# Kernel optimization log

Measured on AMD Instinct MI355X. Metric: run time of the kernel, lower is better.

The kernel has to match this reference:

```python
import jax, jax.numpy as jnp
import numpy as np

N, E, B = 100000, 400000, 4096      # nodes, directed edges, graphs
P, d = 4, 49                        # phm_dim, per-component dim; D = P*d = 196
L = 3                               # message-passing layers
D1, D2 = 64, 32                     # downstream per-component dims (256/4, 128/4)


def setup_inputs():
    key = jax.random.key(0)
    ks = jax.random.split(key, 20)
    def nrm(k, shape, s=0.1):
        return jax.random.normal(k, shape, dtype=jnp.float32) * s
    return {
        "x": jax.random.randint(ks[0], (N, 9), 0, 119),
        "edge_index": jax.random.randint(ks[1], (2, E), 0, N),
        "edge_attr": jax.random.randint(ks[2], (E, 3), 0, 8),
        "batch": jnp.sort(jax.random.randint(ks[3], (N,), 0, B)),
        # encoders: summed categorical embeddings in hypercomplex form [*, P, d]
        "atom_emb": nrm(ks[4], (9, 119, P, d)),
        "bond_emb": nrm(ks[5], (L, 3, 8, P, d)),
        # per-layer PHM conv: contribution matrices A (phm rule) + component weights W
        "conv_A": nrm(ks[6], (L, P, P, P), 0.5),
        "conv_W": nrm(ks[7], (L, P, d, d)),
        "conv_b": jnp.zeros((L, P, d), jnp.float32),
        "mp_gamma": jnp.ones((L, P * d), jnp.float32),
        "mp_beta": jnp.zeros((L, P * d), jnp.float32),
        # soft-attention pooling: PHM linear + real transformer gate
        "pool_A": nrm(ks[8], (P, P, P), 0.5),
        "pool_W": nrm(ks[9], (P, d, d)),
        "pool_b": jnp.zeros((P, d), jnp.float32),
        "pool_rt_w": nrm(ks[10], (P,), 0.5),
        "pool_rt_b": jnp.zeros((d,), jnp.float32),
        # downstream PHM MLP 196 -> 256 -> 128 -> 4*1, then real trafo -> 1
        "dn_A": nrm(ks[11], (3, P, P, P), 0.5),
        "dn1_W": nrm(ks[12], (P, d, D1)),
        "dn1_b": jnp.zeros((P, D1), jnp.float32),
        "dn1_gamma": jnp.ones((P * D1,), jnp.float32),
        "dn1_beta": jnp.zeros((P * D1,), jnp.float32),
        "dn2_W": nrm(ks[13], (P, D1, D2)),
        "dn2_b": jnp.zeros((P, D2), jnp.float32),
        "dn2_gamma": jnp.ones((P * D2,), jnp.float32),
        "dn2_beta": jnp.zeros((P * D2,), jnp.float32),
        "dn3_W": nrm(ks[14], (P, D2, 1)),
        "dn3_b": jnp.zeros((P, 1), jnp.float32),
        "rt_w": nrm(ks[15], (P,), 0.5),
        "rt_b": jnp.zeros((1,), jnp.float32),
    }


def phm_linear(x, A, W, b):
    # PHM linear: y = x @ (sum_i kron(A_i, W_i)) + b, on [n, P, din] -> [n, P, dout]
    return jnp.einsum('nkp,ikj,ipq->njq', x, A, W) + b


def naive_bn(x, gamma, beta, eps=1e-5):
    # naive batch norm over the batch axis, per flattened hypercomplex feature
    n, p, dd = x.shape
    x2 = x.reshape(n, p * dd)
    mu = x2.mean(axis=0)
    var = x2.var(axis=0)
    x2 = (x2 - mu) * jax.lax.rsqrt(var + eps) * gamma + beta
    return x2.reshape(n, p, dd)


def reference(x, edge_index, edge_attr, batch, atom_emb, bond_emb,
              conv_A, conv_W, conv_b, mp_gamma, mp_beta,
              pool_A, pool_W, pool_b, pool_rt_w, pool_rt_b,
              dn_A, dn1_W, dn1_b, dn1_gamma, dn1_beta,
              dn2_W, dn2_b, dn2_gamma, dn2_beta, dn3_W, dn3_b, rt_w, rt_b):
    src, dst = edge_index[0], edge_index[1]
    # atom encoder: sum embeddings of 9 categorical features -> [N, P, d]
    h0 = atom_emb[jnp.arange(9), x].sum(axis=1)
    h = h0
    for l in range(L):  # small fixed layer count
        # bond encoder for this layer -> [E, P, d]
        e = bond_emb[l][jnp.arange(3), edge_attr].sum(axis=1)
        # message = x_j + e_ij (identity msg encoder); self-loop (zero edge feat) adds h
        m = h[src] + e
        agg = jax.ops.segment_sum(m, dst, num_segments=N) + h
        z = phm_linear(agg, conv_A[l], conv_W[l], conv_b[l])
        z = jax.nn.relu(naive_bn(z, mp_gamma[l], mp_beta[l]))
        h = z + h0  # skip-connect to first embedding (sc_type='first')
    # soft-attention pooling: real-valued sigmoid gate per node feature
    g = jax.nn.sigmoid(
        jnp.einsum('npk,p->nk', phm_linear(h, pool_A, pool_W, pool_b), pool_rt_w)
        + pool_rt_b)
    pooled = jax.ops.segment_sum(h * g[:, None, :], batch, num_segments=B)  # [B, P, d]
    # downstream PHM MLP with naive batch norm + relu
    z = jax.nn.relu(naive_bn(phm_linear(pooled, dn_A[0], dn1_W, dn1_b), dn1_gamma, dn1_beta))
    z = jax.nn.relu(naive_bn(phm_linear(z, dn_A[1], dn2_W, dn2_b), dn2_gamma, dn2_beta))
    o = phm_linear(z, dn_A[2], dn3_W, dn3_b)          # [B, P, 1]
    return jnp.einsum('npk,p->nk', o, rt_w) + rt_b    # [B, 1]
```

## Files before the change

kernel.cpp:

```cpp
#include <hip/hip_runtime.h>
#include <cstdint>
#include <cstddef>

#define N_NODES 100000
#define N_EDGES 400000
#define N_GRAPHS 4096
#define DF 196
#define DD 49
#define NPB 5
#define TST 200
#define WSLOT 14336
#define EST 232

#define AS1 __attribute__((address_space(1)))
#define AS3 __attribute__((address_space(3)))

typedef __bf16 bf16x8 __attribute__((ext_vector_type(8)));
typedef float f32x4 __attribute__((ext_vector_type(4)));

__device__ __forceinline__ unsigned short f2bf(float f) {
  unsigned int u = __float_as_uint(f);
  u = u + 0x7FFFu + ((u >> 16) & 1u);
  return (unsigned short)(u >> 16);
}
__device__ __forceinline__ float bf2f(unsigned short h) {
  return __uint_as_float(((unsigned int)h) << 16);
}

__global__ void convert_wfrag_kernel(const float* __restrict__ cA,
                                     const float* __restrict__ cW,
                                     unsigned short* __restrict__ wfrag) {
  int idx = blockIdx.x * blockDim.x + threadIdx.x;
  if (idx >= 3 * 100352) return;
  int l = idx / 100352;
  int r = idx - l * 100352;
  int ct = r / 7168; int r1 = r - ct * 7168;
  int ks = r1 / 1024; int r2 = r1 - ks * 1024;
  int h = r2 / 512;  int r3 = r2 - h * 512;
  int ln = r3 / 8;   int j = r3 - ln * 8;
  int col = ct * 16 + (ln & 15);
  int k = ks * 32 + (ln >> 4) * 8 + j;
  float v = 0.f;
  if (col < DF && k < DF) {
    int k4 = k / DD, p = k - (k / DD) * DD;
    int j4 = col / DD, q = col - (col / DD) * DD;
#pragma unroll
    for (int i = 0; i < 4; i++)
      v += cA[((l * 4 + i) * 4 + k4) * 4 + j4] * cW[((l * 4 + i) * DD + p) * DD + q];
  }
  unsigned short hi = f2bf(v);
  wfrag[idx] = (h == 0) ? hi : f2bf(v - bf2f(hi));
}

__global__ void setup_small_kernel(const float* __restrict__ bond, float* __restrict__ lut,
                                   const float* __restrict__ pA, const float* __restrict__ pW,
                                   const float* __restrict__ pb, const float* __restrict__ rtw,
                                   const float* __restrict__ rtb,
                                   unsigned short* __restrict__ wfragG,
                                   float* __restrict__ gbias,
                                   const float* __restrict__ dnA,
                                   const float* __restrict__ W1, const float* __restrict__ W2,
                                   const float* __restrict__ W3,
                                   float* __restrict__ M1, float* __restrict__ M2,
                                   float* __restrict__ M3) {
  int idx0 = blockIdx.x * blockDim.x + threadIdx.x;
  const int NL = 3 * 512 * DF;
  const int NGF = 28672;
  const int NB2 = 64;
  const int n1 = DF * 256, n2 = 256 * 128, n3 = 128 * 4;
  if (idx0 < NL) {
    int idx = idx0;
    int l = idx / (512 * DF);
    int r = idx - l * (512 * DF);
    int code = r / DF, c = r - (r / DF) * DF;
    int a0 = code & 7, a1 = (code >> 3) & 7, a2 = (code >> 6) & 7;
    lut[idx] = bond[((l * 3 + 0) * 8 + a0) * DF + c]
             + bond[((l * 3 + 1) * 8 + a1) * DF + c]
             + bond[((l * 3 + 2) * 8 + a2) * DF + c];
  } else if (idx0 < NL + NGF) {
    int idx = idx0 - NL;
    int ct = idx / 7168; int r1 = idx - ct * 7168;
    int ks = r1 / 1024; int r2 = r1 - ks * 1024;
    int h = r2 / 512;  int r3 = r2 - h * 512;
    int ln = r3 / 8;   int j = r3 - ln * 8;
    int col = ct * 16 + (ln & 15);
    int k = ks * 32 + (ln >> 4) * 8 + j;
    float v = 0.f;
    if (col < DD && k < DF) {
      int kp = k / DD, p = k - (k / DD) * DD;
#pragma unroll
      for (int i = 0; i < 4; i++) {
        float aw = 0.f;
#pragma unroll
        for (int j4 = 0; j4 < 4; j4++) aw += pA[(i * 4 + kp) * 4 + j4] * rtw[j4];
        v += aw * pW[(i * DD + p) * DD + col];
      }
    }
    unsigned short hi = f2bf(v);
    wfragG[idx] = (h == 0) ? hi : f2bf(v - bf2f(hi));
  } else if (idx0 < NL + NGF + NB2) {
    int q = idx0 - NL - NGF;
    if (q < DD) {
      float s = rtb[q];
#pragma unroll
      for (int j = 0; j < 4; j++) s += rtw[j] * pb[j * DD + q];
      gbias[q] = s;
    }
  } else if (idx0 < NL + NGF + NB2 + n1 + n2 + n3) {
    int idx = idx0 - NL - NGF - NB2;
    if (idx < n1) {
      int r = idx >> 8, c = idx & 255;
      int k = r / DD, p = r - (r / DD) * DD;
      int j = c >> 6, Q = c & 63;
      float s = 0.f;
#pragma unroll
      for (int i = 0; i < 4; i++) s += dnA[i * 16 + k * 4 + j] * W1[(i * DD + p) * 64 + Q];
      M1[idx] = s;
    } else if (idx < n1 + n2) {
      int m = idx - n1;
      int r = m >> 7, c = m & 127;
      int k = r >> 6, p = r & 63, j = c >> 5, q = c & 31;
      float s = 0.f;
#pragma unroll
      for (int i = 0; i < 4; i++) s += dnA[64 + i * 16 + k * 4 + j] * W2[(i * 64 + p) * 32 + q];
      M2[m] = s;
    } else {
      int m = idx - n1 - n2;
      int r = m >> 2, j = m & 3;
      int k = r >> 5, p = r & 31;
      float s = 0.f;
#pragma unroll
      for (int i = 0; i < 4; i++) s += dnA[128 + i * 16 + k * 4 + j] * W3[i * 32 + p];
      M3[m] = s;
    }
  }
}

__global__ void hist_kernel(const int* __restrict__ dst, int* __restrict__ counts) {
  int e = blockIdx.x * blockDim.x + threadIdx.x;
  if (e < N_EDGES) atomicAdd(&counts[dst[e]], 1);
}

__global__ void scan_local_kernel(const int* __restrict__ counts, int* __restrict__ offs,
                                  int* __restrict__ bsum) {
  __shared__ int sm[256];
  int tid = threadIdx.x;
  int gid = blockIdx.x * 256 + tid;
  int v = (gid < N_NODES) ? counts[gid] : 0;
  sm[tid] = v;
  __syncthreads();
  for (int d = 1; d < 256; d <<= 1) {
    int add = (tid >= d) ? sm[tid - d] : 0;
    __syncthreads();
    sm[tid] += add;
    __syncthreads();
  }
  if (gid < N_NODES) offs[gid] = sm[tid] - v;
  if (tid == 255) bsum[blockIdx.x] = sm[255];
}

__global__ void scan_bsum_kernel(int* __restrict__ bsum, int* __restrict__ bpre, int nb) {
  __shared__ int sm[512];
  int tid = threadIdx.x;
  int v = (tid < nb) ? bsum[tid] : 0;
  sm[tid] = v;
  __syncthreads();
  for (int d = 1; d < 512; d <<= 1) {
    int add = (tid >= d) ? sm[tid - d] : 0;
    __syncthreads();
    sm[tid] += add;
    __syncthreads();
  }
  if (tid < nb) bpre[tid] = sm[tid] - v;
}

__global__ void add_off_kernel(int* __restrict__ offs, const int* __restrict__ bpre) {
  int gid = blockIdx.x * blockDim.x + threadIdx.x;
  if (gid < N_NODES) offs[gid] += bpre[gid >> 8];
  if (gid == 0) offs[N_NODES] = N_EDGES;
}

__global__ void scatter_kernel(const int* __restrict__ src, const int* __restrict__ dst,
                               const int* __restrict__ ea, int* __restrict__ counts,
                               const int* __restrict__ offs,
                               unsigned int* __restrict__ sorted) {
  int e = blockIdx.x * blockDim.x + threadIdx.x;
  if (e >= N_EDGES) return;
  int d = dst[e];
  int code = ea[e * 3 + 0] | (ea[e * 3 + 1] << 3) | (ea[e * 3 + 2] << 6);
  int pos = offs[d] + atomicSub(&counts[d], 1) - 1;
  sorted[pos] = (unsigned int)src[e] | ((unsigned int)code << 17);
}

__global__ void sortseg_kernel(const int* __restrict__ offs,
                               unsigned int* __restrict__ sorted) {
  int n = blockIdx.x * blockDim.x + threadIdx.x;
  if (n >= N_NODES) return;
  int s = offs[n], e = offs[n + 1];
  for (int i = s + 1; i < e; i++) {
    unsigned int v = sorted[i];
    int j = i - 1;
    while (j >= s && sorted[j] > v) { sorted[j + 1] = sorted[j]; j--; }
    sorted[j + 1] = v;
  }
}

__global__ void atom_enc_kernel(const int* __restrict__ x, const float* __restrict__ emb,
                                float* __restrict__ h0) {
  int idx = blockIdx.x * blockDim.x + threadIdx.x;
  if (idx >= N_NODES * DF) return;
  int n = idx / DF;
  int c = idx - n * DF;
  float s = 0.f;
#pragma unroll
  for (int f = 0; f < 9; f++) {
    int xi = x[n * 9 + f];
    s += emb[(f * 119 + xi) * DF + c];
  }
  h0[idx] = s;
}

__global__ __launch_bounds__(256)
void agg_kernel(const float* __restrict__ h, const int* __restrict__ offs,
                const unsigned int* __restrict__ sorted, const float* __restrict__ lut,
                unsigned short* __restrict__ tH, unsigned short* __restrict__ tL) {
  int t = threadIdx.x;
  int i = t / 49, q = t - i * 49;
  if (i >= NPB) return;
  int node = blockIdx.x * NPB + i;
  if (node >= N_NODES) return;
  const float4* h4 = (const float4*)h;
  const float4* l4 = (const float4*)lut;
  float4 acc = h4[(size_t)node * 49 + q];
  int s = offs[node], e = offs[node + 1];
  for (int k = s; k < e; k++) {
    unsigned int se = sorted[k];
    int srcn = se & 0x1FFFF;
    int code = se >> 17;
    float4 hv = h4[(size_t)srcn * 49 + q];
    float4 lv = l4[(size_t)code * 49 + q];
    acc.x += hv.x + lv.x;
    acc.y += hv.y + lv.y;
    acc.z += hv.z + lv.z;
    acc.w += hv.w + lv.w;
  }
  ushort4 hh, ll;
  hh.x = f2bf(acc.x); ll.x = f2bf(acc.x - bf2f(hh.x));
  hh.y = f2bf(acc.y); ll.y = f2bf(acc.y - bf2f(hh.y));
  hh.z = f2bf(acc.z); ll.z = f2bf(acc.z - bf2f(hh.z));
  hh.w = f2bf(acc.w); ll.w = f2bf(acc.w - bf2f(hh.w));
  size_t ob = (size_t)node * TST + q * 4;
  *(ushort4*)(tH + ob) = hh;
  *(ushort4*)(tL + ob) = ll;
  if (q == 48) {
    ushort4 z = make_ushort4(0, 0, 0, 0);
    *(ushort4*)(tH + (size_t)node * TST + 196) = z;
    *(ushort4*)(tL + (size_t)node * TST + 196) = z;
  }
}

__global__ __launch_bounds__(256, 2)
void conv_mfma_kernel(unsigned short* __restrict__ tH,
                      unsigned short* __restrict__ tL,
                      const unsigned short* __restrict__ wfrag,
                      const float* __restrict__ bias,
                      float* __restrict__ stats) {
  __shared__ __align__(16) unsigned short smW[2 * 64 * EST];
  const int t = threadIdx.x;
  const int lane = t & 63;
  const int w = t >> 6;
  const int li = lane & 15;
  const int rg = lane >> 4;
  const int rowbase = blockIdx.x * 128 + w * 32;

  f32x4 acc[2][14];
#pragma unroll
  for (int rt = 0; rt < 2; rt++)
#pragma unroll
    for (int ct = 0; ct < 14; ct++) acc[rt][ct] = (f32x4){0.f, 0.f, 0.f, 0.f};

  uint4 b0h[2], b0l[2], b1h[2], b1l[2], b2h[2], b2l[2], b3h[2], b3l[2];

#define LOADA(ks, aH, aL)                                                      \
  {                                                                            \
    _Pragma("unroll") for (int rt = 0; rt < 2; rt++) {                         \
      size_t o = (size_t)(rowbase + rt * 16 + li) * TST + (ks) * 32 + rg * 8;  \
      aH[rt] = *(const uint4*)(tH + o);                                        \
      aL[rt] = *(const uint4*)(tL + o);                                        \
    }                                                                          \
  }

#define WLOAD(ks, sbase)                                                       \
  {                                                                            \
    _Pragma("unroll") for (int f0 = 0; f0 < 7; f0++) {                         \
      int g = f0 * 4 + w;                                                      \
      int hh = g & 1, ct = g >> 1;                                             \
      __builtin_amdgcn_global_load_lds(                                        \
          (AS1 const void*)(wfrag + ((size_t)(ct * 7 + (ks)) * 2 + hh) * 512 + lane * 8), \
          (AS3 void*)(smW + (sbase) + (ct * 2 + hh) * 512), 16, 0, 0);         \
    }                                                                          \
  }

#define COMPUTE(sbase, aH, aL)                                                 \
  {                                                                            \
    _Pragma("unroll") for (int ct = 0; ct < 14; ct++) {                        \
      bf16x8 bh = *(const bf16x8*)(smW + (sbase) + ((ct * 2 + 0) * 512 + lane * 8)); \
      bf16x8 bl = *(const bf16x8*)(smW + (sbase) + ((ct * 2 + 1) * 512 + lane * 8)); \
      _Pragma("unroll") for (int rt = 0; rt < 2; rt++) {                       \
        bf16x8 ah = *(const bf16x8*)&aH[rt];                                   \
        bf16x8 al = *(const bf16x8*)&aL[rt];                                   \
        acc[rt][ct] = __builtin_amdgcn_mfma_f32_16x16x32_bf16(ah, bh, acc[rt][ct], 0, 0, 0); \
        acc[rt][ct] = __builtin_amdgcn_mfma_f32_16x16x32_bf16(al, bh, acc[rt][ct], 0, 0, 0); \
        acc[rt][ct] = __builtin_amdgcn_mfma_f32_16x16x32_bf16(ah, bl, acc[rt][ct], 0, 0, 0); \
      }                                                                        \
    }                                                                          \
  }

#define BARC(N)                                                                \
  {                                                                            \
    asm volatile("s_waitcnt vmcnt(" #N ")" ::: "memory");                      \
    __builtin_amdgcn_s_barrier();                                              \
  }
#define PINW() __builtin_amdgcn_sched_barrier(0)

  WLOAD(0, 0);
  PINW();
  LOADA(0, b0h, b0l);
  LOADA(1, b1h, b1l);
  LOADA(2, b2h, b2l);
  BARC(12);
  WLOAD(1, WSLOT); PINW(); LOADA(3, b3h, b3l); COMPUTE(0, b0h, b0l);     BARC(4);
  WLOAD(2, 0);     PINW(); LOADA(4, b0h, b0l); COMPUTE(WSLOT, b1h, b1l); BARC(4);
  WLOAD(3, WSLOT); PINW(); LOADA(5, b1h, b1l); COMPUTE(0, b2h, b2l);     BARC(4);
  WLOAD(4, 0);     PINW(); LOADA(6, b2h, b2l); COMPUTE(WSLOT, b3h, b3l); BARC(4);
  WLOAD(5, WSLOT); PINW();                     COMPUTE(0, b0h, b0l);     BARC(0);
  WLOAD(6, 0);     PINW();                     COMPUTE(WSLOT, b1h, b1l); BARC(0);
  COMPUTE(0, b2h, b2l);

  float part[14], psq[14];
#pragma unroll
  for (int ct = 0; ct < 14; ct++) { part[ct] = 0.f; psq[ct] = 0.f; }

  unsigned short* lhi = smW;
  unsigned short* llo = smW + 64 * EST;

#pragma unroll
  for (int half = 0; half < 2; half++) {
    __syncthreads();
    if ((w >> 1) == half) {
      int rl0 = (w & 1) * 32;
#pragma unroll
      for (int ct = 0; ct < 14; ct++) {
        int c = ct * 16 + li;
        float bv = (c < DF) ? bias[c] : 0.f;
#pragma unroll
        for (int rt = 0; rt < 2; rt++) {
#pragma unroll
          for (int r = 0; r < 4; r++) {
            int row = rl0 + rt * 16 + rg * 4 + r;
            int gr = rowbase + rt * 16 + rg * 4 + r;
            float y = acc[rt][ct][r] + bv;
            if (gr < N_NODES && c < DF) { part[ct] += y; psq[ct] += y * y; }
            unsigned short hi = f2bf(y);
            lhi[row * EST + c] = hi;
            llo[row * EST + c] = f2bf(y - bf2f(hi));
          }
        }
      }
    }
    __syncthreads();
    for (int idx = t; idx < 1600; idx += 256) {
      int row = idx / 25, u = idx - (idx / 25) * 25;
      int gr = blockIdx.x * 128 + half * 64 + row;
      if (gr < N_NODES) {
        uint4 vh = *(const uint4*)(lhi + row * EST + u * 8);
        uint4 vl = *(const uint4*)(llo + row * EST + u * 8);
        if (u == 24) { vh.z = 0u; vh.w = 0u; vl.z = 0u; vl.w = 0u; }
        *(uint4*)(tH + (size_t)gr * TST + u * 8) = vh;
        *(uint4*)(tL + (size_t)gr * TST + u * 8) = vl;
      }
    }
  }

  __syncthreads();
  float* redS = (float*)smW;
  float* redQ = redS + 4 * 224;
#pragma unroll
  for (int ct = 0; ct < 14; ct++) {
    float p = part[ct], q = psq[ct];
    p += __shfl_xor(p, 16, 64); p += __shfl_xor(p, 32, 64);
    q += __shfl_xor(q, 16, 64); q += __shfl_xor(q, 32, 64);
    if (rg == 0) { redS[w * 224 + ct * 16 + li] = p; redQ[w * 224 + ct * 16 + li] = q; }
  }
  __syncthreads();
  if (t < DF) {
    float s1 = redS[t] + redS[224 + t] + redS[448 + t] + redS[672 + t];
    float s2 = redQ[t] + redQ[224 + t] + redQ[448 + t] + redQ[672 + t];
    atomicAdd(&stats[t], s1);
    atomicAdd(&stats[DF + t], s2);
  }
#undef LOADA
#undef WLOAD
#undef COMPUTE
#undef BARC
#undef PINW
}

__global__ void bn_relu_split_kernel(unsigned short* __restrict__ tH,
                                     unsigned short* __restrict__ tL,
                                     const float* __restrict__ stats,
                                     const float* __restrict__ gamma,
                                     const float* __restrict__ beta,
                                     const float* __restrict__ h0,
                                     float* __restrict__ h, int write_split) {
  int idx = blockIdx.x * blockDim.x + threadIdx.x;
  if (idx >= N_NODES * DD) return;
  int n = idx / DD, q = idx - (idx / DD) * DD;
  size_t ib = (size_t)n * TST + q * 4;
  ushort4 hv = *(const ushort4*)(tH + ib);
  ushort4 lv = *(const ushort4*)(tL + ib);
  size_t fb = (size_t)n * DF + q * 4;
  float4 sk = *(const float4*)(h0 + fb);
  int c = q * 4;
  const float invN = 1.f / N_NODES;
  float4 o;
  {
    float z = bf2f(hv.x) + bf2f(lv.x);
    float mu = stats[c + 0] * invN;
    float var = stats[DF + c + 0] * invN - mu * mu;
    o.x = fmaxf((z - mu) * rsqrtf(var + 1e-5f) * gamma[c + 0] + beta[c + 0], 0.f) + sk.x;
  }
  {
    float z = bf2f(hv.y) + bf2f(lv.y);
    float mu = stats[c + 1] * invN;
    float var = stats[DF + c + 1] * invN - mu * mu;
    o.y = fmaxf((z - mu) * rsqrtf(var + 1e-5f) * gamma[c + 1] + beta[c + 1], 0.f) + sk.y;
  }
  {
    float z = bf2f(hv.z) + bf2f(lv.z);
    float mu = stats[c + 2] * invN;
    float var = stats[DF + c + 2] * invN - mu * mu;
    o.z = fmaxf((z - mu) * rsqrtf(var + 1e-5f) * gamma[c + 2] + beta[c + 2], 0.f) + sk.z;
  }
  {
    float z = bf2f(hv.w) + bf2f(lv.w);
    float mu = stats[c + 3] * invN;
    float var = stats[DF + c + 3] * invN - mu * mu;
    o.w = fmaxf((z - mu) * rsqrtf(var + 1e-5f) * gamma[c + 3] + beta[c + 3], 0.f) + sk.w;
  }
  *(float4*)(h + fb) = o;
  if (write_split) {
    ushort4 sh, sl;
    sh.x = f2bf(o.x); sl.x = f2bf(o.x - bf2f(sh.x));
    sh.y = f2bf(o.y); sl.y = f2bf(o.y - bf2f(sh.y));
    sh.z = f2bf(o.z); sl.z = f2bf(o.z - bf2f(sh.z));
    sh.w = f2bf(o.w); sl.w = f2bf(o.w - bf2f(sh.w));
    *(ushort4*)(tH + ib) = sh;
    *(ushort4*)(tL + ib) = sl;
  }
}

__global__ __launch_bounds__(256, 2)
void gate_mfma_kernel(const unsigned short* __restrict__ tH,
                      const unsigned short* __restrict__ tL,
                      const unsigned short* __restrict__ wfragG,
                      const float* __restrict__ gbias,
                      float* __restrict__ g) {
  __shared__ __align__(16) unsigned short smW[28672];
  const int t = threadIdx.x;
  const int lane = t & 63;
  const int w = t >> 6;
  const int li = lane & 15;
  const int rg = lane >> 4;
  const int rowbase = blockIdx.x * 128 + w * 32;

  f32x4 acc[2][4];
#pragma unroll
  for (int rt = 0; rt < 2; rt++)
#pragma unroll
    for (int ct = 0; ct < 4; ct++) acc[rt][ct] = (f32x4){0.f, 0.f, 0.f, 0.f};

  uint4 b0h[2], b0l[2], b1h[2], b1l[2], b2h[2], b2l[2], b3h[2], b3l[2];

#define LOADA(ks, aH, aL)                                                      \
  {                                                                            \
    _Pragma("unroll") for (int rt = 0; rt < 2; rt++) {                         \
      size_t o = (size_t)(rowbase + rt * 16 + li) * TST + (ks) * 32 + rg * 8;  \
      aH[rt] = *(const uint4*)(tH + o);                                        \
      aL[rt] = *(const uint4*)(tL + o);                                        \
    }                                                                          \
  }

#define COMPUTE(ks, aH, aL)                                                    \
  {                                                                            \
    _Pragma("unroll") for (int ct = 0; ct < 4; ct++) {                         \
      bf16x8 bh = *(const bf16x8*)(smW + ((ct * 7 + (ks)) * 2 + 0) * 512 + lane * 8); \
      bf16x8 bl = *(const bf16x8*)(smW + ((ct * 7 + (ks)) * 2 + 1) * 512 + lane * 8); \
      _Pragma("unroll") for (int rt = 0; rt < 2; rt++) {                       \
        bf16x8 ah = *(const bf16x8*)&aH[rt];                                   \
        bf16x8 al = *(const bf16x8*)&aL[rt];                                   \
        acc[rt][ct] = __builtin_amdgcn_mfma_f32_16x16x32_bf16(ah, bh, acc[rt][ct], 0, 0, 0); \
        acc[rt][ct] = __builtin_amdgcn_mfma_f32_16x16x32_bf16(al, bh, acc[rt][ct], 0, 0, 0); \
        acc[rt][ct] = __builtin_amdgcn_mfma_f32_16x16x32_bf16(ah, bl, acc[rt][ct], 0, 0, 0); \
      }                                                                        \
    }                                                                          \
  }

  LOADA(0, b0h, b0l);
  LOADA(1, b1h, b1l);
  LOADA(2, b2h, b2l);
  for (int i = t; i < 3584; i += 256)
    *(uint4*)(smW + (size_t)i * 8) = *(const uint4*)(wfragG + (size_t)i * 8);
  __syncthreads();
  LOADA(3, b3h, b3l); COMPUTE(0, b0h, b0l);
  LOADA(4, b0h, b0l); COMPUTE(1, b1h, b1l);
  LOADA(5, b1h, b1l); COMPUTE(2, b2h, b2l);
  LOADA(6, b2h, b2l); COMPUTE(3, b3h, b3l);
  COMPUTE(4, b0h, b0l);
  COMPUTE(5, b1h, b1l);
  COMPUTE(6, b2h, b2l);

#pragma unroll
  for (int ct = 0; ct < 4; ct++) {
    int c = ct * 16 + li;
    if (c < DD) {
      float bv = gbias[c];
#pragma unroll
      for (int rt = 0; rt < 2; rt++) {
#pragma unroll
        for (int r = 0; r < 4; r++) {
          int gr = rowbase + rt * 16 + rg * 4 + r;
          if (gr < N_NODES) {
            float v = acc[rt][ct][r] + bv;
            g[(size_t)gr * DD + c] = 1.f / (1.f + __expf(-v));
          }
        }
      }
    }
  }
#undef LOADA
#undef COMPUTE
}

template<int S, int MODE>
__launch_bounds__(256)
__global__ void gemm_kernel(const float* X, const float* __restrict__ W,
                            const float* __restrict__ bias, float* Y,
                            float* __restrict__ stats, int Nrows, int K, int NC) {
  constexpr int WN = S * 64;
  __shared__ __align__(16) float At[32][64];
  __shared__ __align__(16) float Wl[32][WN];
  const int t = threadIdx.x;
  const int tx = t & 15;
  const int ty = t >> 4;
  const int r0 = blockIdx.x * 64;

  float acc[S][4][4];
#pragma unroll
  for (int s = 0; s < S; s++)
#pragma unroll
    for (int i = 0; i < 4; i++)
#pragma unroll
      for (int j = 0; j < 4; j++) acc[s][i][j] = 0.f;

  const int lr = t >> 2;
  const int kb = (t & 3) * 8;
  constexpr int TPR = S * 16;
  const int cw = (t % TPR) * 4;
  const int kr = t / TPR;
  constexpr int RPP = 256 / TPR;
  constexpr int PASSES = 32 / RPP;

  for (int k0 = 0; k0 < K; k0 += 32) {
    {
      const int gr = r0 + lr;
      const float* xp = X + (size_t)gr * K + k0 + kb;
      if (gr < Nrows && (k0 + kb + 7) < K) {
        float4 v0 = *(const float4*)(xp);
        float4 v1 = *(const float4*)(xp + 4);
        At[kb + 0][lr] = v0.x; At[kb + 1][lr] = v0.y;
        At[kb + 2][lr] = v0.z; At[kb + 3][lr] = v0.w;
        At[kb + 4][lr] = v1.x; At[kb + 5][lr] = v1.y;
        At[kb + 6][lr] = v1.z; At[kb + 7][lr] = v1.w;
      } else {
#pragma unroll
        for (int i = 0; i < 8; i++) {
          int kk = kb + i;
          float v = 0.f;
          if (gr < Nrows && (k0 + kk) < K) v = xp[i];
          At[kk][lr] = v;
        }
      }
    }
#pragma unroll
    for (int ps = 0; ps < PASSES; ps++) {
      int kk = kr + ps * RPP;
      int gk = k0 + kk;
      if (gk < K && (cw + 3) < NC && ((NC & 3) == 0)) {
        float4 v = *(const float4*)(W + (size_t)gk * NC + cw);
        Wl[kk][cw + 0] = v.x; Wl[kk][cw + 1] = v.y;
        Wl[kk][cw + 2] = v.z; Wl[kk][cw + 3] = v.w;
      } else {
#pragma unroll
        for (int j = 0; j < 4; j++) {
          int c = cw + j;
          float v = 0.f;
          if (gk < K && c < NC) v = W[(size_t)gk * NC + c];
          Wl[kk][c] = v;
        }
      }
    }
    __syncthreads();
#pragma unroll 4
    for (int kk = 0; kk < 32; kk++) {
      float4 a = *(const float4*)&At[kk][ty * 4];
      float av[4] = {a.x, a.y, a.z, a.w};
#pragma unroll
      for (int s = 0; s < S; s++) {
        float4 w = *(const float4*)&Wl[kk][s * 64 + tx * 4];
        float wv[4] = {w.x, w.y, w.z, w.w};
#pragma unroll
        for (int i = 0; i < 4; i++)
#pragma unroll
          for (int j = 0; j < 4; j++)
            acc[s][i][j] = fmaf(av[i], wv[j], acc[s][i][j]);
      }
    }
    __syncthreads();
  }

#pragma unroll
  for (int s = 0; s < S; s++)
#pragma unroll
    for (int j = 0; j < 4; j++) {
      int c = s * 64 + tx * 4 + j;
      float bv = (c < NC) ? bias[c] : 0.f;
#pragma unroll
      for (int i = 0; i < 4; i++) {
        float y = acc[s][i][j] + bv;
        if (MODE == 1) y = 1.f / (1.f + __expf(-y));
        acc[s][i][j] = y;
      }
    }
#pragma unroll
  for (int i = 0; i < 4; i++) {
    int gr = r0 + ty * 4 + i;
    if (gr < Nrows) {
#pragma unroll
      for (int s = 0; s < S; s++)
#pragma unroll
        for (int j = 0; j < 4; j++) {
          int c = s * 64 + tx * 4 + j;
          if (c < NC) Y[(size_t)gr * NC + c] = acc[s][i][j];
        }
    }
  }
  if (MODE == 0) {
    float* red = &Wl[0][0];
    __syncthreads();
#pragma unroll
    for (int s = 0; s < S; s++)
#pragma unroll
      for (int j = 0; j < 4; j++) {
        float p = 0.f;
#pragma unroll
        for (int i = 0; i < 4; i++)
          if ((r0 + ty * 4 + i) < Nrows) p += acc[s][i][j];
        red[ty * WN + s * 64 + tx * 4 + j] = p;
      }
    __syncthreads();
    if (t < WN) {
      float tot = 0.f;
#pragma unroll
      for (int yy = 0; yy < 16; yy++) tot += red[yy * WN + t];
      if (t < NC) atomicAdd(&stats[t], tot);
    }
    __syncthreads();
#pragma unroll
    for (int s = 0; s < S; s++)
#pragma unroll
      for (int j = 0; j < 4; j++) {
        float p = 0.f;
#pragma unroll
        for (int i = 0; i < 4; i++)
          if ((r0 + ty * 4 + i) < Nrows) p += acc[s][i][j] * acc[s][i][j];
        red[ty * WN + s * 64 + tx * 4 + j] = p;
      }
    __syncthreads();
    if (t < WN) {
      float tot = 0.f;
#pragma unroll
      for (int yy = 0; yy < 16; yy++) tot += red[yy * WN + t];
      if (t < NC) atomicAdd(&stats[NC + t], tot);
    }
  }
}

__global__ void bn_relu_kernel(const float* __restrict__ z, const float* __restrict__ stats,
                               const float* __restrict__ gamma, const float* __restrict__ beta,
                               float* __restrict__ out,
                               int total, int NC, float invN) {
  int idx = blockIdx.x * blockDim.x + threadIdx.x;
  if (idx >= total) return;
  int c = idx % NC;
  float mu = stats[c] * invN;
  float var = stats[NC + c] * invN - mu * mu;
  float v = (z[idx] - mu) * rsqrtf(var + 1e-5f) * gamma[c] + beta[c];
  out[idx] = fmaxf(v, 0.f);
}

__device__ __forceinline__ int lower_bound_dev(const int* a, int n, int v) {
  int lo = 0, hi = n;
  while (lo < hi) { int mid = (lo + hi) >> 1; if (a[mid] < v) lo = mid + 1; else hi = mid; }
  return lo;
}

__global__ void pool_kernel(const float* __restrict__ h, const float* __restrict__ g,
                            const int* __restrict__ batch, float* __restrict__ pooled) {
  int b = blockIdx.x;
  __shared__ int bounds[2];
  if (threadIdx.x == 0) {
    bounds[0] = lower_bound_dev(batch, N_NODES, b);
    bounds[1] = lower_bound_dev(batch, N_NODES, b + 1);
  }
  __syncthreads();
  int c = threadIdx.x;
  if (c >= DF) return;
  int s = bounds[0], e = bounds[1];
  int q = c % DD;
  float acc = 0.f;
  for (int n = s; n < e; n++)
    acc = fmaf(h[(size_t)n * DF + c], g[(size_t)n * DD + q], acc);
  pooled[(size_t)b * DF + c] = acc;
}

__global__ void final_kernel(const float* __restrict__ z2, const float* __restrict__ M3,
                             const float* __restrict__ b3, const float* __restrict__ rtw,
                             const float* __restrict__ rtb, float* __restrict__ out) {
  __shared__ float sM[128 * 4];
  __shared__ float srw[4];
  __shared__ float srb;
  int t = threadIdx.x;
  for (int i = t; i < 512; i += 256) sM[i] = M3[i];
  if (t < 4) srw[t] = rtw[t];
  if (t == 4) srb = rtb[0];
  __syncthreads();
  int b = blockIdx.x * blockDim.x + t;
  if (b >= N_GRAPHS) return;
  float o0 = b3[0], o1 = b3[1], o2 = b3[2], o3 = b3[3];
  const float* zp = z2 + (size_t)b * 128;
  for (int p = 0; p < 128; p++) {
    float v = zp[p];
    o0 = fmaf(v, sM[p * 4 + 0], o0);
    o1 = fmaf(v, sM[p * 4 + 1], o1);
    o2 = fmaf(v, sM[p * 4 + 2], o2);
    o3 = fmaf(v, sM[p * 4 + 3], o3);
  }
  out[b] = srb + o0 * srw[0] + o1 * srw[1] + o2 * srw[2] + o3 * srw[3];
}

extern "C" void kernel_launch(void* const* d_in, const int* in_sizes, int n_in,
                              void* d_out, int out_size, void* d_ws, size_t ws_size,
                              hipStream_t stream) {
  (void)in_sizes; (void)n_in; (void)out_size; (void)ws_size;
  const int* x          = (const int*)d_in[0];
  const int* edge_index = (const int*)d_in[1];
  const int* edge_attr  = (const int*)d_in[2];
  const int* batch      = (const int*)d_in[3];
  const float* atom_emb = (const float*)d_in[4];
  const float* bond_emb = (const float*)d_in[5];
  const float* conv_A   = (const float*)d_in[6];
  const float* conv_W   = (const float*)d_in[7];
  const float* conv_b   = (const float*)d_in[8];
  const float* mp_gamma = (const float*)d_in[9];
  const float* mp_beta  = (const float*)d_in[10];
  const float* pool_A   = (const float*)d_in[11];
  const float* pool_W   = (const float*)d_in[12];
  const float* pool_b   = (const float*)d_in[13];
  const float* pool_rt_w = (const float*)d_in[14];
  const float* pool_rt_b = (const float*)d_in[15];
  const float* dn_A     = (const float*)d_in[16];
  const float* dn1_W    = (const float*)d_in[17];
  const float* dn1_b    = (const float*)d_in[18];
  const float* dn1_gamma = (const float*)d_in[19];
  const float* dn1_beta = (const float*)d_in[20];
  const float* dn2_W    = (const float*)d_in[21];
  const float* dn2_b    = (const float*)d_in[22];
  const float* dn2_gamma = (const float*)d_in[23];
  const float* dn2_beta = (const float*)d_in[24];
  const float* dn3_W    = (const float*)d_in[25];
  const float* dn3_b    = (const float*)d_in[26];
  const float* rt_w     = (const float*)d_in[27];
  const float* rt_b     = (const float*)d_in[28];
  float* out = (float*)d_out;

  char* ws = (char*)d_ws;
  size_t off = 0;
  auto alloc = [&](size_t bytes) -> char* {
    char* p = ws + off;
    off = (off + bytes + 255) & ~(size_t)255;
    return p;
  };
  const size_t HBYTES = (size_t)N_NODES * DF * sizeof(float);
  float* h0 = (float*)alloc(HBYTES);
  float* h  = (float*)alloc(HBYTES);
  unsigned short* tH = (unsigned short*)alloc((size_t)N_NODES * TST * 2 + 4096);
  unsigned short* tL = (unsigned short*)alloc((size_t)N_NODES * TST * 2 + 4096);
  float* g      = (float*)h0;
  float* pooled = (float*)((char*)h0 + (((size_t)N_NODES * DD * 4 + 255) & ~(size_t)255));
  float* z1     = (float*)((char*)pooled + (((size_t)N_GRAPHS * DF * 4 + 255) & ~(size_t)255));
  float* z2     = (float*)((char*)z1 + (((size_t)N_GRAPHS * 256 * 4 + 255) & ~(size_t)255));
  unsigned short* wfrag = (unsigned short*)alloc((size_t)3 * 100352 * 2);
  unsigned short* wfragG = (unsigned short*)alloc((size_t)28672 * 2);
  float* gbias  = (float*)alloc(64 * 4);
  float* M1     = (float*)alloc(DF * 256 * 4);
  float* M2     = (float*)alloc(256 * 128 * 4);
  float* M3     = (float*)alloc(128 * 4 * 4);
  float* stats  = (float*)alloc(2048 * 4);
  int*  counts  = (int*)alloc(N_NODES * 4);
  int*  offs    = (int*)alloc((N_NODES + 1) * 4);
  unsigned int* sorted = (unsigned int*)alloc((size_t)N_EDGES * 4);
  float* lut    = (float*)alloc((size_t)3 * 512 * DF * 4);
  int*  bsum    = (int*)alloc(512 * 4);
  int*  bpre    = (int*)alloc(512 * 4);

  const int* src = edge_index;
  const int* dst = edge_index + N_EDGES;
  const int NB = (N_NODES + 255) / 256;

  hipMemsetAsync(stats, 0, 2048 * 4, stream);
  hipMemsetAsync(counts, 0, N_NODES * 4, stream);

  convert_wfrag_kernel<<<(3 * 100352 + 255) / 256, 256, 0, stream>>>(conv_A, conv_W, wfrag);
  {
    const int total = 3 * 512 * DF + 28672 + 64 + (DF * 256 + 256 * 128 + 128 * 4);
    setup_small_kernel<<<(total + 255) / 256, 256, 0, stream>>>(
        bond_emb, lut, pool_A, pool_W, pool_b, pool_rt_w, pool_rt_b, wfragG, gbias,
        dn_A, dn1_W, dn2_W, dn3_W, M1, M2, M3);
  }

  hist_kernel<<<(N_EDGES + 255) / 256, 256, 0, stream>>>(dst, counts);
  scan_local_kernel<<<NB, 256, 0, stream>>>(counts, offs, bsum);
  scan_bsum_kernel<<<1, 512, 0, stream>>>(bsum, bpre, NB);
  add_off_kernel<<<NB, 256, 0, stream>>>(offs, bpre);
  scatter_kernel<<<(N_EDGES + 255) / 256, 256, 0, stream>>>(
      src, dst, edge_attr, counts, offs, sorted);
  sortseg_kernel<<<NB, 256, 0, stream>>>(offs, sorted);

  atom_enc_kernel<<<(N_NODES * DF + 255) / 256, 256, 0, stream>>>(x, atom_emb, h0);

  const int NCONV = (N_NODES + 127) / 128;
  for (int l = 0; l < 3; l++) {
    const float* hl = (l == 0) ? h0 : h;
    agg_kernel<<<(N_NODES + NPB - 1) / NPB, 256, 0, stream>>>(
        hl, offs, sorted, lut + (size_t)l * 512 * DF, tH, tL);
    float* st = stats + l * 392;
    conv_mfma_kernel<<<NCONV, 256, 0, stream>>>(
        tH, tL, wfrag + (size_t)l * 100352, conv_b + (size_t)l * DF, st);
    bn_relu_split_kernel<<<(N_NODES * DD + 255) / 256, 256, 0, stream>>>(
        tH, tL, st, mp_gamma + l * DF, mp_beta + l * DF, h0, h, (l == 2) ? 1 : 0);
  }

  gate_mfma_kernel<<<NCONV, 256, 0, stream>>>(tH, tL, wfragG, gbias, g);
  pool_kernel<<<N_GRAPHS, 256, 0, stream>>>(h, g, batch, pooled);

  gemm_kernel<4, 0><<<(N_GRAPHS + 63) / 64, 256, 0, stream>>>(
      pooled, M1, dn1_b, z1, stats + 1176, N_GRAPHS, DF, 256);
  bn_relu_kernel<<<(N_GRAPHS * 256 + 255) / 256, 256, 0, stream>>>(
      z1, stats + 1176, dn1_gamma, dn1_beta, z1, N_GRAPHS * 256, 256, 1.f / N_GRAPHS);
  gemm_kernel<2, 0><<<(N_GRAPHS + 63) / 64, 256, 0, stream>>>(
      z1, M2, dn2_b, z2, stats + 1688, N_GRAPHS, 256, 128);
  bn_relu_kernel<<<(N_GRAPHS * 128 + 255) / 256, 256, 0, stream>>>(
      z2, stats + 1688, dn2_gamma, dn2_beta, z2, N_GRAPHS * 128, 128, 1.f / N_GRAPHS);
  final_kernel<<<(N_GRAPHS + 255) / 256, 256, 0, stream>>>(z2, M3, dn3_b, rt_w, rt_b, out);
}
```

Baseline: 875.8 us.

## Single-buffer weight LDS in PHM GEMM, unroll edge aggregation by two

The GEMM kernel drops the double-buffered LDS weight slots and uses one slot. Each k-step now loads, waits, barriers, computes, then barriers again before the next load. Shrinking the epilogue stride (EST 232→200) together with the single slot cuts LDS use, so more blocks can be resident. The cost is that the weight load no longer overlaps with compute. The aggregation kernel's edge loop is unrolled by two so more independent gathers are in flight.

```diff
diff --git a/kernel.cpp b/kernel.cpp
--- a/kernel.cpp
+++ b/kernel.cpp
@@ -9,8 +9,7 @@
 #define DD 49
 #define NPB 5
 #define TST 200
-#define WSLOT 14336
-#define EST 232
+#define EST 200
 
 #define AS1 __attribute__((address_space(1)))
 #define AS3 __attribute__((address_space(3)))
@@ -233,7 +232,22 @@
   const float4* l4 = (const float4*)lut;
   float4 acc = h4[(size_t)node * 49 + q];
   int s = offs[node], e = offs[node + 1];
-  for (int k = s; k < e; k++) {
+  int k = s;
+  for (; k + 2 <= e; k += 2) {
+    unsigned int se0 = sorted[k];
+    unsigned int se1 = sorted[k + 1];
+    int s0 = se0 & 0x1FFFF, c0 = se0 >> 17;
+    int s1 = se1 & 0x1FFFF, c1 = se1 >> 17;
+    float4 hv0 = h4[(size_t)s0 * 49 + q];
+    float4 lv0 = l4[(size_t)c0 * 49 + q];
+    float4 hv1 = h4[(size_t)s1 * 49 + q];
+    float4 lv1 = l4[(size_t)c1 * 49 + q];
+    acc.x += (hv0.x + lv0.x) + (hv1.x + lv1.x);
+    acc.y += (hv0.y + lv0.y) + (hv1.y + lv1.y);
+    acc.z += (hv0.z + lv0.z) + (hv1.z + lv1.z);
+    acc.w += (hv0.w + lv0.w) + (hv1.w + lv1.w);
+  }
+  if (k < e) {
     unsigned int se = sorted[k];
     int srcn = se & 0x1FFFF;
     int code = se >> 17;
@@ -290,22 +304,22 @@
     }                                                                          \
   }
 
-#define WLOAD(ks, sbase)                                                       \
+#define WLOAD(ks)                                                              \
   {                                                                            \
     _Pragma("unroll") for (int f0 = 0; f0 < 7; f0++) {                         \
       int g = f0 * 4 + w;                                                      \
       int hh = g & 1, ct = g >> 1;                                             \
       __builtin_amdgcn_global_load_lds(                                        \
           (AS1 const void*)(wfrag + ((size_t)(ct * 7 + (ks)) * 2 + hh) * 512 + lane * 8), \
-          (AS3 void*)(smW + (sbase) + (ct * 2 + hh) * 512), 16, 0, 0);         \
+          (AS3 void*)(smW + (ct * 2 + hh) * 512), 16, 0, 0);                   \
     }                                                                          \
   }
 
-#define COMPUTE(sbase, aH, aL)                                                 \
+#define COMPUTE(aH, aL)                                                        \
   {                                                                            \
     _Pragma("unroll") for (int ct = 0; ct < 14; ct++) {                        \
-      bf16x8 bh = *(const bf16x8*)(smW + (sbase) + ((ct * 2 + 0) * 512 + lane * 8)); \
-      bf16x8 bl = *(const bf16x8*)(smW + (sbase) + ((ct * 2 + 1) * 512 + lane * 8)); \
+      bf16x8 bh = *(const bf16x8*)(smW + ((ct * 2 + 0) * 512 + lane * 8));     \
+      bf16x8 bl = *(const bf16x8*)(smW + ((ct * 2 + 1) * 512 + lane * 8));     \
       _Pragma("unroll") for (int rt = 0; rt < 2; rt++) {                       \
         bf16x8 ah = *(const bf16x8*)&aH[rt];                                   \
         bf16x8 al = *(const bf16x8*)&aL[rt];                                   \
@@ -316,26 +330,43 @@
     }                                                                          \
   }
 
-#define BARC(N)                                                                \
+#define BARW(N)                                                                \
   {                                                                            \
     asm volatile("s_waitcnt vmcnt(" #N ")" ::: "memory");                      \
     __builtin_amdgcn_s_barrier();                                              \
   }
+#define BARL()                                                                 \
+  {                                                                            \
+    asm volatile("s_waitcnt lgkmcnt(0)" ::: "memory");                         \
+    __builtin_amdgcn_s_barrier();                                              \
+  }
 #define PINW() __builtin_amdgcn_sched_barrier(0)
 
-  WLOAD(0, 0);
+  WLOAD(0);
   PINW();
   LOADA(0, b0h, b0l);
   LOADA(1, b1h, b1l);
   LOADA(2, b2h, b2l);
-  BARC(12);
-  WLOAD(1, WSLOT); PINW(); LOADA(3, b3h, b3l); COMPUTE(0, b0h, b0l);     BARC(4);
-  WLOAD(2, 0);     PINW(); LOADA(4, b0h, b0l); COMPUTE(WSLOT, b1h, b1l); BARC(4);
-  WLOAD(3, WSLOT); PINW(); LOADA(5, b1h, b1l); COMPUTE(0, b2h, b2l);     BARC(4);
-  WLOAD(4, 0);     PINW(); LOADA(6, b2h, b2l); COMPUTE(WSLOT, b3h, b3l); BARC(4);
-  WLOAD(5, WSLOT); PINW();                     COMPUTE(0, b0h, b0l);     BARC(0);
-  WLOAD(6, 0);     PINW();                     COMPUTE(WSLOT, b1h, b1l); BARC(0);
-  COMPUTE(0, b2h, b2l);
+  BARW(12);
+  COMPUTE(b0h, b0l);
+  BARL();
+  WLOAD(1); PINW(); LOADA(3, b3h, b3l); BARW(4);
+  COMPUTE(b1h, b1l);
+  BARL();
+  WLOAD(2); PINW(); LOADA(4, b0h, b0l); BARW(4);
+  COMPUTE(b2h, b2l);
+  BARL();
+  WLOAD(3); PINW(); LOADA(5, b1h, b1l); BARW(4);
+  COMPUTE(b3h, b3l);
+  BARL();
+  WLOAD(4); PINW(); LOADA(6, b2h, b2l); BARW(4);
+  COMPUTE(b0h, b0l);
+  BARL();
+  WLOAD(5); PINW(); BARW(0);
+  COMPUTE(b1h, b1l);
+  BARL();
+  WLOAD(6); PINW(); BARW(0);
+  COMPUTE(b2h, b2l);
 
   float part[14], psq[14];
 #pragma unroll
@@ -361,9 +392,11 @@
             int gr = rowbase + rt * 16 + rg * 4 + r;
             float y = acc[rt][ct][r] + bv;
             if (gr < N_NODES && c < DF) { part[ct] += y; psq[ct] += y * y; }
-            unsigned short hi = f2bf(y);
-            lhi[row * EST + c] = hi;
-            llo[row * EST + c] = f2bf(y - bf2f(hi));
+            if (c < DF) {
+              unsigned short hi = f2bf(y);
+              lhi[row * EST + c] = hi;
+              llo[row * EST + c] = f2bf(y - bf2f(hi));
+            }
           }
         }
       }
@@ -402,7 +435,8 @@
 #undef LOADA
 #undef WLOAD
 #undef COMPUTE
-#undef BARC
+#undef BARW
+#undef BARL
 #undef PINW
 }
 
```

Result: no change. 870.5 us (-0.6%).

## Split conv GEMM across column halves and write fp32 output into h

Applied to the files above, without the earlier changes.

The conv MFMA kernel now launches two blocks per 128-row tile, each computing half of the output columns (7 of 14 column tiles). This halves the accumulator registers and LDS per block and doubles the block count. The conv output is now written as fp32 directly into h instead of as bf16 hi/lo pairs into tH/tL, and the BN kernel reads it back from h, so the split conversion moves out of the conv epilogue. The agg loop is also unrolled by two to raise memory-level parallelism. Each A tile is now loaded twice, once per column half, which adds A-operand traffic.

```diff
diff --git a/kernel.cpp b/kernel.cpp
--- a/kernel.cpp
+++ b/kernel.cpp
@@ -9,8 +9,8 @@
 #define DD 49
 #define NPB 5
 #define TST 200
-#define WSLOT 14336
-#define EST 232
+#define WSLOT2 7168
+#define ESTF 116
 
 #define AS1 __attribute__((address_space(1)))
 #define AS3 __attribute__((address_space(3)))
@@ -233,7 +233,22 @@
   const float4* l4 = (const float4*)lut;
   float4 acc = h4[(size_t)node * 49 + q];
   int s = offs[node], e = offs[node + 1];
-  for (int k = s; k < e; k++) {
+  int k = s;
+  for (; k + 2 <= e; k += 2) {
+    unsigned int se0 = sorted[k];
+    unsigned int se1 = sorted[k + 1];
+    int s0 = se0 & 0x1FFFF, c0 = se0 >> 17;
+    int s1 = se1 & 0x1FFFF, c1 = se1 >> 17;
+    float4 hv0 = h4[(size_t)s0 * 49 + q];
+    float4 lv0 = l4[(size_t)c0 * 49 + q];
+    float4 hv1 = h4[(size_t)s1 * 49 + q];
+    float4 lv1 = l4[(size_t)c1 * 49 + q];
+    acc.x += (hv0.x + lv0.x) + (hv1.x + lv1.x);
+    acc.y += (hv0.y + lv0.y) + (hv1.y + lv1.y);
+    acc.z += (hv0.z + lv0.z) + (hv1.z + lv1.z);
+    acc.w += (hv0.w + lv0.w) + (hv1.w + lv1.w);
+  }
+  if (k < e) {
     unsigned int se = sorted[k];
     int srcn = se & 0x1FFFF;
     int code = se >> 17;
@@ -260,24 +275,28 @@
 }
 
 __global__ __launch_bounds__(256, 2)
-void conv_mfma_kernel(unsigned short* __restrict__ tH,
-                      unsigned short* __restrict__ tL,
+void conv_mfma_kernel(const unsigned short* __restrict__ tH,
+                      const unsigned short* __restrict__ tL,
                       const unsigned short* __restrict__ wfrag,
                       const float* __restrict__ bias,
+                      float* __restrict__ zout,
                       float* __restrict__ stats) {
-  __shared__ __align__(16) unsigned short smW[2 * 64 * EST];
+  __shared__ __align__(16) unsigned short smW[14848];
   const int t = threadIdx.x;
   const int lane = t & 63;
   const int w = t >> 6;
   const int li = lane & 15;
   const int rg = lane >> 4;
-  const int rowbase = blockIdx.x * 128 + w * 32;
-
-  f32x4 acc[2][14];
+  const int rb = blockIdx.x >> 1;
+  const int ch = blockIdx.x & 1;
+  const int rowbase = rb * 128 + w * 32;
+  const unsigned short* wsrc = wfrag + (size_t)ch * 7 * 7168;
+
+  f32x4 acc[2][7];
 #pragma unroll
   for (int rt = 0; rt < 2; rt++)
 #pragma unroll
-    for (int ct = 0; ct < 14; ct++) acc[rt][ct] = (f32x4){0.f, 0.f, 0.f, 0.f};
+    for (int ct = 0; ct < 7; ct++) acc[rt][ct] = (f32x4){0.f, 0.f, 0.f, 0.f};
 
   uint4 b0h[2], b0l[2], b1h[2], b1l[2], b2h[2], b2l[2], b3h[2], b3l[2];
 
@@ -292,18 +311,20 @@
 
 #define WLOAD(ks, sbase)                                                       \
   {                                                                            \
-    _Pragma("unroll") for (int f0 = 0; f0 < 7; f0++) {                         \
+    _Pragma("unroll") for (int f0 = 0; f0 < 4; f0++) {                         \
       int g = f0 * 4 + w;                                                      \
-      int hh = g & 1, ct = g >> 1;                                             \
-      __builtin_amdgcn_global_load_lds(                                        \
-          (AS1 const void*)(wfrag + ((size_t)(ct * 7 + (ks)) * 2 + hh) * 512 + lane * 8), \
-          (AS3 void*)(smW + (sbase) + (ct * 2 + hh) * 512), 16, 0, 0);         \
+      if (g < 14) {                                                            \
+        int hh = g & 1, ct = g >> 1;                                           \
+        __builtin_amdgcn_global_load_lds(                                      \
+            (AS1 const void*)(wsrc + ((size_t)(ct * 7 + (ks)) * 2 + hh) * 512 + lane * 8), \
+            (AS3 void*)(smW + (sbase) + (ct * 2 + hh) * 512), 16, 0, 0);       \
+      }                                                                        \
     }                                                                          \
   }
 
 #define COMPUTE(sbase, aH, aL)                                                 \
   {                                                                            \
-    _Pragma("unroll") for (int ct = 0; ct < 14; ct++) {                        \
+    _Pragma("unroll") for (int ct = 0; ct < 7; ct++) {                         \
       bf16x8 bh = *(const bf16x8*)(smW + (sbase) + ((ct * 2 + 0) * 512 + lane * 8)); \
       bf16x8 bl = *(const bf16x8*)(smW + (sbase) + ((ct * 2 + 1) * 512 + lane * 8)); \
       _Pragma("unroll") for (int rt = 0; rt < 2; rt++) {                       \
@@ -329,20 +350,20 @@
   LOADA(1, b1h, b1l);
   LOADA(2, b2h, b2l);
   BARC(12);
-  WLOAD(1, WSLOT); PINW(); LOADA(3, b3h, b3l); COMPUTE(0, b0h, b0l);     BARC(4);
-  WLOAD(2, 0);     PINW(); LOADA(4, b0h, b0l); COMPUTE(WSLOT, b1h, b1l); BARC(4);
-  WLOAD(3, WSLOT); PINW(); LOADA(5, b1h, b1l); COMPUTE(0, b2h, b2l);     BARC(4);
-  WLOAD(4, 0);     PINW(); LOADA(6, b2h, b2l); COMPUTE(WSLOT, b3h, b3l); BARC(4);
-  WLOAD(5, WSLOT); PINW();                     COMPUTE(0, b0h, b0l);     BARC(0);
-  WLOAD(6, 0);     PINW();                     COMPUTE(WSLOT, b1h, b1l); BARC(0);
+  WLOAD(1, WSLOT2); PINW(); LOADA(3, b3h, b3l); COMPUTE(0, b0h, b0l);      BARC(4);
+  WLOAD(2, 0);      PINW(); LOADA(4, b0h, b0l); COMPUTE(WSLOT2, b1h, b1l); BARC(4);
+  WLOAD(3, WSLOT2); PINW(); LOADA(5, b1h, b1l); COMPUTE(0, b2h, b2l);      BARC(4);
+  WLOAD(4, 0);      PINW(); LOADA(6, b2h, b2l); COMPUTE(WSLOT2, b3h, b3l); BARC(4);
+  WLOAD(5, WSLOT2); PINW();                     COMPUTE(0, b0h, b0l);      BARC(0);
+  WLOAD(6, 0);      PINW();                     COMPUTE(WSLOT2, b1h, b1l); BARC(0);
   COMPUTE(0, b2h, b2l);
 
-  float part[14], psq[14];
-#pragma unroll
-  for (int ct = 0; ct < 14; ct++) { part[ct] = 0.f; psq[ct] = 0.f; }
-
-  unsigned short* lhi = smW;
-  unsigned short* llo = smW + 64 * EST;
+  float part[7], psq[7];
+#pragma unroll
+  for (int ct = 0; ct < 7; ct++) { part[ct] = 0.f; psq[ct] = 0.f; }
+
+  float* lz = (float*)smW;
+  const int NU = ch ? 21 : 28;
 
 #pragma unroll
   for (int half = 0; half < 2; half++) {
@@ -350,9 +371,10 @@
     if ((w >> 1) == half) {
       int rl0 = (w & 1) * 32;
 #pragma unroll
-      for (int ct = 0; ct < 14; ct++) {
-        int c = ct * 16 + li;
-        float bv = (c < DF) ? bias[c] : 0.f;
+      for (int ct = 0; ct < 7; ct++) {
+        int cl = ct * 16 + li;
+        int cg = ch * 112 + cl;
+        float bv = (cg < DF) ? bias[cg] : 0.f;
 #pragma unroll
         for (int rt = 0; rt < 2; rt++) {
 #pragma unroll
@@ -360,44 +382,42 @@
             int row = rl0 + rt * 16 + rg * 4 + r;
             int gr = rowbase + rt * 16 + rg * 4 + r;
             float y = acc[rt][ct][r] + bv;
-            if (gr < N_NODES && c < DF) { part[ct] += y; psq[ct] += y * y; }
-            unsigned short hi = f2bf(y);
-            lhi[row * EST + c] = hi;
-            llo[row * EST + c] = f2bf(y - bf2f(hi));
+            if (gr < N_NODES && cg < DF) { part[ct] += y; psq[ct] += y * y; }
+            lz[row * ESTF + cl] = y;
           }
         }
       }
     }
     __syncthreads();
-    for (int idx = t; idx < 1600; idx += 256) {
-      int row = idx / 25, u = idx - (idx / 25) * 25;
-      int gr = blockIdx.x * 128 + half * 64 + row;
+    for (int idx = t; idx < 64 * NU; idx += 256) {
+      int row = idx / NU, u = idx - (idx / NU) * NU;
+      int gr = rb * 128 + half * 64 + row;
       if (gr < N_NODES) {
-        uint4 vh = *(const uint4*)(lhi + row * EST + u * 8);
-        uint4 vl = *(const uint4*)(llo + row * EST + u * 8);
-        if (u == 24) { vh.z = 0u; vh.w = 0u; vl.z = 0u; vl.w = 0u; }
-        *(uint4*)(tH + (size_t)gr * TST + u * 8) = vh;
-        *(uint4*)(tL + (size_t)gr * TST + u * 8) = vl;
+        float4 v = *(const float4*)(lz + row * ESTF + u * 4);
+        *(float4*)(zout + (size_t)gr * DF + ch * 112 + u * 4) = v;
       }
     }
   }
 
   __syncthreads();
   float* redS = (float*)smW;
-  float* redQ = redS + 4 * 224;
-#pragma unroll
-  for (int ct = 0; ct < 14; ct++) {
+  float* redQ = redS + 4 * 112;
+#pragma unroll
+  for (int ct = 0; ct < 7; ct++) {
     float p = part[ct], q = psq[ct];
     p += __shfl_xor(p, 16, 64); p += __shfl_xor(p, 32, 64);
     q += __shfl_xor(q, 16, 64); q += __shfl_xor(q, 32, 64);
-    if (rg == 0) { redS[w * 224 + ct * 16 + li] = p; redQ[w * 224 + ct * 16 + li] = q; }
+    if (rg == 0) { redS[w * 112 + ct * 16 + li] = p; redQ[w * 112 + ct * 16 + li] = q; }
   }
   __syncthreads();
-  if (t < DF) {
-    float s1 = redS[t] + redS[224 + t] + redS[448 + t] + redS[672 + t];
-    float s2 = redQ[t] + redQ[224 + t] + redQ[448 + t] + redQ[672 + t];
-    atomicAdd(&stats[t], s1);
-    atomicAdd(&stats[DF + t], s2);
+  if (t < 112) {
+    int cg = ch * 112 + t;
+    if (cg < DF) {
+      float s1 = redS[t] + redS[112 + t] + redS[224 + t] + redS[336 + t];
+      float s2 = redQ[t] + redQ[112 + t] + redQ[224 + t] + redQ[336 + t];
+      atomicAdd(&stats[cg], s1);
+      atomicAdd(&stats[DF + cg], s2);
+    }
   }
 #undef LOADA
 #undef WLOAD
@@ -406,50 +426,46 @@
 #undef PINW
 }
 
-__global__ void bn_relu_split_kernel(unsigned short* __restrict__ tH,
-                                     unsigned short* __restrict__ tL,
-                                     const float* __restrict__ stats,
+__global__ void bn_relu_split_kernel(const float* __restrict__ stats,
                                      const float* __restrict__ gamma,
                                      const float* __restrict__ beta,
                                      const float* __restrict__ h0,
-                                     float* __restrict__ h, int write_split) {
+                                     float* __restrict__ h,
+                                     unsigned short* __restrict__ tH,
+                                     unsigned short* __restrict__ tL,
+                                     int write_split) {
   int idx = blockIdx.x * blockDim.x + threadIdx.x;
   if (idx >= N_NODES * DD) return;
   int n = idx / DD, q = idx - (idx / DD) * DD;
-  size_t ib = (size_t)n * TST + q * 4;
-  ushort4 hv = *(const ushort4*)(tH + ib);
-  ushort4 lv = *(const ushort4*)(tL + ib);
   size_t fb = (size_t)n * DF + q * 4;
+  float4 zv = *(const float4*)(h + fb);
   float4 sk = *(const float4*)(h0 + fb);
   int c = q * 4;
   const float invN = 1.f / N_NODES;
   float4 o;
   {
-    float z = bf2f(hv.x) + bf2f(lv.x);
     float mu = stats[c + 0] * invN;
     float var = stats[DF + c + 0] * invN - mu * mu;
-    o.x = fmaxf((z - mu) * rsqrtf(var + 1e-5f) * gamma[c + 0] + beta[c + 0], 0.f) + sk.x;
+    o.x = fmaxf((zv.x - mu) * rsqrtf(var + 1e-5f) * gamma[c + 0] + beta[c + 0], 0.f) + sk.x;
   }
   {
-    float z = bf2f(hv.y) + bf2f(lv.y);
     float mu = stats[c + 1] * invN;
     float var = stats[DF + c + 1] * invN - mu * mu;
-    o.y = fmaxf((z - mu) * rsqrtf(var + 1e-5f) * gamma[c + 1] + beta[c + 1], 0.f) + sk.y;
+    o.y = fmaxf((zv.y - mu) * rsqrtf(var + 1e-5f) * gamma[c + 1] + beta[c + 1], 0.f) + sk.y;
   }
   {
-    float z = bf2f(hv.z) + bf2f(lv.z);
     float mu = stats[c + 2] * invN;
     float var = stats[DF + c + 2] * invN - mu * mu;
-    o.z = fmaxf((z - mu) * rsqrtf(var + 1e-5f) * gamma[c + 2] + beta[c + 2], 0.f) + sk.z;
+    o.z = fmaxf((zv.z - mu) * rsqrtf(var + 1e-5f) * gamma[c + 2] + beta[c + 2], 0.f) + sk.z;
   }
   {
-    float z = bf2f(hv.w) + bf2f(lv.w);
     float mu = stats[c + 3] * invN;
     float var = stats[DF + c + 3] * invN - mu * mu;
-    o.w = fmaxf((z - mu) * rsqrtf(var + 1e-5f) * gamma[c + 3] + beta[c + 3], 0.f) + sk.w;
+    o.w = fmaxf((zv.w - mu) * rsqrtf(var + 1e-5f) * gamma[c + 3] + beta[c + 3], 0.f) + sk.w;
   }
   *(float4*)(h + fb) = o;
   if (write_split) {
+    size_t ib = (size_t)n * TST + q * 4;
     ushort4 sh, sl;
     sh.x = f2bf(o.x); sl.x = f2bf(o.x - bf2f(sh.x));
     sh.y = f2bf(o.y); sl.y = f2bf(o.y - bf2f(sh.y));
@@ -849,19 +865,20 @@
 
   atom_enc_kernel<<<(N_NODES * DF + 255) / 256, 256, 0, stream>>>(x, atom_emb, h0);
 
-  const int NCONV = (N_NODES + 127) / 128;
+  const int NROW = (N_NODES + 127) / 128;
+  const int NCONV = NROW * 2;
   for (int l = 0; l < 3; l++) {
     const float* hl = (l == 0) ? h0 : h;
     agg_kernel<<<(N_NODES + NPB - 1) / NPB, 256, 0, stream>>>(
         hl, offs, sorted, lut + (size_t)l * 512 * DF, tH, tL);
     float* st = stats + l * 392;
     conv_mfma_kernel<<<NCONV, 256, 0, stream>>>(
-        tH, tL, wfrag + (size_t)l * 100352, conv_b + (size_t)l * DF, st);
+        tH, tL, wfrag + (size_t)l * 100352, conv_b + (size_t)l * DF, h, st);
     bn_relu_split_kernel<<<(N_NODES * DD + 255) / 256, 256, 0, stream>>>(
-        tH, tL, st, mp_gamma + l * DF, mp_beta + l * DF, h0, h, (l == 2) ? 1 : 0);
-  }
-
-  gate_mfma_kernel<<<NCONV, 256, 0, stream>>>(tH, tL, wfragG, gbias, g);
+        st, mp_gamma + l * DF, mp_beta + l * DF, h0, h, tH, tL, (l == 2) ? 1 : 0);
+  }
+
+  gate_mfma_kernel<<<NROW, 256, 0, stream>>>(tH, tL, wfragG, gbias, g);
   pool_kernel<<<N_GRAPHS, 256, 0, stream>>>(h, g, batch, pooled);
 
   gemm_kernel<4, 0><<<(N_GRAPHS + 63) / 64, 256, 0, stream>>>(
```

Result: faster. 851.2 us (-2.8%).
